# Performance work log

Measured on AMD Instinct MI355X. Metric: run time of the kernel, lower is better.

The kernel has to match this reference:

```python
import jax, jax.numpy as jnp
import numpy as np

B, S, DIMS, HEAD = 4, 4096, 1024, 16
HD = DIMS // HEAD


def setup_inputs() -> dict:
    key = jax.random.key(0)
    ks = jax.random.split(key, 9)
    inv = 1.0 / np.sqrt(DIMS)
    return {
        "x": jax.random.normal(ks[0], (B, S, DIMS), dtype=jnp.float32),
        "Wq": jax.random.normal(ks[1], (DIMS, DIMS), dtype=jnp.float32) * inv,
        "bq": jax.random.normal(ks[2], (DIMS,), dtype=jnp.float32) * 0.02,
        "Wk": jax.random.normal(ks[3], (DIMS, DIMS), dtype=jnp.float32) * inv,
        "bk": jax.random.normal(ks[4], (DIMS,), dtype=jnp.float32) * 0.02,
        "Wv": jax.random.normal(ks[5], (DIMS, DIMS), dtype=jnp.float32) * inv,
        "bv": jax.random.normal(ks[6], (DIMS,), dtype=jnp.float32) * 0.02,
        "Wo": jax.random.normal(ks[7], (DIMS, DIMS), dtype=jnp.float32) * inv,
        "bo": jax.random.normal(ks[8], (DIMS,), dtype=jnp.float32) * 0.02,
        "skip_pattern": 4,
    }


def reference(x, Wq, bq, Wk, bk, Wv, bv, Wo, bo, skip_pattern):
    b, s, _ = x.shape
    scale = DIMS ** (-0.5)  # NOTE: source scales by full dims, not head_dim

    def proj(W, bias):
        # torch Linear: x @ W.T + b ; then [B,S,H,HD] -> [B,H,S,HD]
        y = jnp.einsum('bsd,ed->bse', x, W) + bias
        return y.reshape(b, s, HEAD, HD).transpose(0, 2, 1, 3)

    q = proj(Wq, bq)
    k = proj(Wk, bk)
    v = proj(Wv, bv)

    # strided KV downsample (static python-int stride -> static shapes under jit)
    k_s = k[:, :, ::skip_pattern, :]  # [B,H,S//skip,HD]
    v_s = v[:, :, ::skip_pattern, :]

    scores = jnp.einsum('bhqd,bhkd->bhqk', q, k_s) * scale
    attn = jax.nn.softmax(scores, axis=-1)
    out = jnp.einsum('bhqk,bhkd->bhqd', attn, v_s)  # [B,H,S,HD]
    out = out.transpose(0, 2, 1, 3).reshape(b, s, DIMS)
    return jnp.einsum('bsd,ed->bse', out, Wo) + bo
```

## Files before the change

### kernel.cpp

```cpp
#include <hip/hip_runtime.h>
#include <hip/hip_bf16.h>
#include <stdint.h>


using short8 = short __attribute__((ext_vector_type(8)));
using f32x4  = float __attribute__((ext_vector_type(4)));
using f32x16 = float __attribute__((ext_vector_type(16)));

#define MFMA16(A,B,C) __builtin_amdgcn_mfma_f32_16x16x32_bf16((A),(B),(C),0,0,0)
#define MFMA32(A,B,C) __builtin_amdgcn_mfma_f32_32x32x16_bf16((A),(B),(C),0,0,0)

#define QSC 0.0450842200277800f

#define VT_OFF 4194304

__device__ __forceinline__ unsigned short f2bf(float f) {
  unsigned int x = __float_as_uint(f);
  x += 0x7fffu + ((x >> 16) & 1u);
  return (unsigned short)(x >> 16);
}

__device__ __forceinline__ unsigned pack2(float a, float b) {
  float2 t; t.x = a; t.y = b;
  union { __hip_bfloat162 h; unsigned u; } cv;
  cv.h = __float22bfloat162_rn(t);
  return cv.u;
}

__device__ __forceinline__ float fexp2(float x) {
  float r; asm("v_exp_f32 %0, %1" : "=v"(r) : "v"(x)); return r;
}

#define PLSWAP(a,b) asm volatile("v_permlane32_swap_b32 %0, %1" : "+v"(a), "+v"(b))

__device__ __forceinline__ void gld_lds16(const void* g, void* l) {
  __builtin_amdgcn_global_load_lds(
      (const __attribute__((address_space(1))) void*)g,
      (__attribute__((address_space(3))) void*)l,
      16, 0, 0);
}

__global__ __launch_bounds__(256) void cvtall_kernel(
    const float* __restrict__ x,  unsigned short* __restrict__ xb,
    const float* __restrict__ w0, const float* __restrict__ w1,
    const float* __restrict__ w2, const float* __restrict__ w3,
    unsigned short* __restrict__ o0, unsigned short* __restrict__ o1,
    unsigned short* __restrict__ o2, unsigned short* __restrict__ o3) {
  int bid = blockIdx.x, tid = threadIdx.x;
  const float* in; unsigned short* out; int n4, i0, stride;
  if (bid < 2048) {
    in = x; out = xb; n4 = 4194304; i0 = bid * 256 + tid; stride = 2048 * 256;
  } else {
    int t = (bid - 2048) >> 7;
    switch (t) {
      case 0: in = w0; out = o0; break;
      case 1: in = w1; out = o1; break;
      case 2: in = w2; out = o2; break;
      default: in = w3; out = o3; break;
    }
    n4 = 262144; i0 = ((bid - 2048) & 127) * 256 + tid; stride = 128 * 256;
  }
  for (int i = i0; i < n4; i += stride) {
    float4 v = ((const float4*)in)[i];
    ushort4 o;
    o.x = f2bf(v.x); o.y = f2bf(v.y); o.z = f2bf(v.z); o.w = f2bf(v.w);
    ((ushort4*)out)[i] = o;
  }
}

template<int MODE, int ROWMUL>
__device__ __forceinline__ void gemm_body(
    unsigned short* __restrict__ lA, unsigned short* __restrict__ lB,
    const unsigned short* __restrict__ A,
    const unsigned short* __restrict__ W,
    const float* __restrict__ biasA,
    const float* __restrict__ biasB,
    void* __restrict__ outp,
    int NB, int bid, int nwg)
{
  constexpr int K = 1024;
  int vid = (bid & 7) * (nwg >> 3) + (bid >> 3);
  int bm = vid / NB, bn = vid % NB;

  int tid = threadIdx.x;
  int w = tid >> 6, l = tid & 63;
  int wm = w >> 1, wn = w & 1;
  int fr = l & 15, fk = l >> 4;

  int sr = w * 16 + (l >> 2);
  int sc = ((l & 3) ^ ((l >> 3) & 3)) * 8;
  const unsigned short* ga0 = A + (size_t)ROWMUL * (size_t)(bm * 128 + sr) * K + sc;
  const unsigned short* ga1 = A + (size_t)ROWMUL * (size_t)(bm * 128 + 64 + sr) * K + sc;
  const unsigned short* gb0 = W + (size_t)(bn * 128 + sr) * K + sc;
  const unsigned short* gb1 = W + (size_t)(bn * 128 + 64 + sr) * K + sc;
  unsigned short* la0 = &lA[(w * 16) * 32];
  unsigned short* la1 = &lA[(64 + w * 16) * 32];
  unsigned short* lb0 = &lB[(w * 16) * 32];
  unsigned short* lb1 = &lB[(64 + w * 16) * 32];

  int physk = (fk ^ ((fr >> 1) & 3)) * 8;

  f32x4 acc[4][4];
  #pragma unroll
  for (int i = 0; i < 4; ++i)
    #pragma unroll
    for (int j = 0; j < 4; ++j) acc[i][j] = (f32x4){0.f, 0.f, 0.f, 0.f};

  for (int kt = 0; kt < K / 64; ++kt) {
    gld_lds16(ga0 + kt * 64,      la0);
    gld_lds16(ga0 + kt * 64 + 32, la0 + 4096);
    gld_lds16(ga1 + kt * 64,      la1);
    gld_lds16(ga1 + kt * 64 + 32, la1 + 4096);
    gld_lds16(gb0 + kt * 64,      lb0);
    gld_lds16(gb0 + kt * 64 + 32, lb0 + 4096);
    gld_lds16(gb1 + kt * 64,      lb1);
    gld_lds16(gb1 + kt * 64 + 32, lb1 + 4096);
    __syncthreads();
    #pragma unroll
    for (int kh = 0; kh < 2; ++kh) {
      int base = kh * 4096;
      short8 af[4], bf[4];
      #pragma unroll
      for (int mi = 0; mi < 4; ++mi)
        af[mi] = *(const short8*)&lA[base + (wm * 64 + mi * 16 + fr) * 32 + physk];
      #pragma unroll
      for (int nj = 0; nj < 4; ++nj)
        bf[nj] = *(const short8*)&lB[base + (wn * 64 + nj * 16 + fr) * 32 + physk];
      __builtin_amdgcn_s_setprio(1);
      #pragma unroll
      for (int mi = 0; mi < 4; ++mi)
        #pragma unroll
        for (int nj = 0; nj < 4; ++nj)
          acc[mi][nj] = MFMA16(af[mi], bf[nj], acc[mi][nj]);
      __builtin_amdgcn_s_setprio(0);
    }
    __syncthreads();
  }

  float bv[4];
  #pragma unroll
  for (int nj = 0; nj < 4; ++nj) {
    int n = bn * 128 + wn * 64 + nj * 16 + fr;
    bv[nj] = (MODE == 4) ? (n < 1024 ? biasA[n] : biasB[n - 1024]) : biasA[n];
  }

  #pragma unroll
  for (int mi = 0; mi < 4; ++mi) {
    #pragma unroll
    for (int nj = 0; nj < 4; ++nj) {
      #pragma unroll
      for (int j = 0; j < 4; ++j) {
        int m = bm * 128 + wm * 64 + mi * 16 + fk * 4 + j;
        int n = bn * 128 + wn * 64 + nj * 16 + fr;
        float v = acc[mi][nj][j] + bv[nj];
        if (MODE == 0) {
          ((float*)outp)[(size_t)m * 1024 + n] = v;
        } else if (MODE == 1) {
          size_t idx = (size_t)((m >> 12) * 16 + (n >> 6)) * 262144
                     + (size_t)(m & 4095) * 64 + (n & 63);
          ((unsigned short*)outp)[idx] = f2bf(v * QSC);
        } else {
          if (n < 1024) {
            size_t idx = (size_t)((m >> 10) * 16 + (n >> 6)) * 65536
                       + (size_t)(m & 1023) * 64 + (n & 63);
            ((unsigned short*)outp)[idx] = f2bf(v);
          } else {
            int nn = n - 1024;
            size_t idx = (size_t)VT_OFF
                       + (size_t)((m >> 10) * 16 + (nn >> 6)) * 65536
                       + (size_t)(nn & 63) * 1024 + (m & 1023);
            ((unsigned short*)outp)[idx] = f2bf(v);
          }
        }
      }
    }
  }
}

__global__ __launch_bounds__(256) void proj_fused_kernel(
    const unsigned short* __restrict__ xb,
    const unsigned short* __restrict__ wqb,
    const unsigned short* __restrict__ wkb,
    const float* __restrict__ bq,
    const float* __restrict__ bk,
    const float* __restrict__ bv,
    unsigned short* __restrict__ qb,
    unsigned short* __restrict__ kb)
{
  __shared__ unsigned short lA[128 * 64];
  __shared__ unsigned short lB[128 * 64];
  int bid = blockIdx.x;
  if (bid < 1024) {
    gemm_body<1, 1>(lA, lB, xb, wqb, bq, bq, qb, 8, bid, 1024);
  } else {
    gemm_body<4, 4>(lA, lB, xb, wkb, bk, bv, kb, 16, bid - 1024, 512);
  }
}

__global__ __launch_bounds__(256) void oproj_kernel(
    const unsigned short* __restrict__ ab,
    const unsigned short* __restrict__ wob,
    const float* __restrict__ bo,
    float* __restrict__ out)
{
  __shared__ unsigned short lA[128 * 64];
  __shared__ unsigned short lB[128 * 64];
  gemm_body<0, 1>(lA, lB, ab, wob, bo, bo, out, 8, blockIdx.x, 1024);
}

__global__ __launch_bounds__(512) void attn_kernel(
    const unsigned short* __restrict__ Q,
    const unsigned short* __restrict__ Ks,
    const unsigned short* __restrict__ Vt,
    unsigned short* __restrict__ O)
{
  __shared__ unsigned short lds[16384];
  unsigned short* lsK = lds;
  unsigned short* lsV = lds + 8192;

  int bid = blockIdx.x;
  int vid = (bid & 7) * 128 + (bid >> 3);
  int bh = vid >> 4;
  int qt = vid & 15;
  int tid = threadIdx.x;
  int w = tid >> 6, l = tid & 63;
  int l31 = l & 31, hi = l >> 5;
  int q0 = qt * 256 + w * 32;

  short8 qf[4];
  {
    const unsigned short* qp = Q + ((size_t)bh * 4096 + q0 + l31) * 64 + hi * 8;
    #pragma unroll
    for (int s = 0; s < 4; ++s) qf[s] = *(const short8*)(qp + s * 16);
  }

  const unsigned short* Kbh = Ks + (size_t)bh * 65536;
  const unsigned short* Vbh = Vt + (size_t)bh * 65536;

  int r = w * 8 + (l >> 3);
  int c0 = ((l & 7) ^ (l >> 3)) * 8;
  int dst = w * 512;

#define STAGE(BUF, KC)                                                          \
  {                                                                             \
    const unsigned short* Kb = Kbh + (KC) * 4096;                               \
    const unsigned short* Vb = Vbh + (KC) * 64;                                 \
    gld_lds16(Kb + r * 64 + c0, &lsK[(BUF) * 4096 + dst]);                      \
    gld_lds16(Vb + (size_t)r * 1024 + c0, &lsV[(BUF) * 4096 + dst]);            \
  }

  float lrun = 0.f;
  f32x16 oa0, oa1;
  #pragma unroll
  for (int rr = 0; rr < 16; ++rr) { oa0[rr] = 0.f; oa1[rr] = 0.f; }

  STAGE(0, 0);
  __syncthreads();

  int rb0 = l31 * 64, rb1 = rb0 + 2048;
  int rsw = l31 & 7;

  for (int kc = 0; kc < 16; ++kc) {
    int b = kc & 1;
    if (kc + 1 < 16) STAGE(b ^ 1, kc + 1);

    const unsigned short* Kl = &lsK[b * 4096];
    const unsigned short* Vl = &lsV[b * 4096];

    f32x16 s0, s1;
    #pragma unroll
    for (int rr = 0; rr < 16; ++rr) { s0[rr] = 0.f; s1[rr] = 0.f; }
    __builtin_amdgcn_s_setprio(1);
    #pragma unroll
    for (int s = 0; s < 4; ++s) {
      int co = ((hi + 2 * s) ^ rsw) * 8;
      short8 kf0 = *(const short8*)&Kl[rb0 + co];
      short8 kf1 = *(const short8*)&Kl[rb1 + co];
      s0 = MFMA32(kf0, qf[s], s0);
      s1 = MFMA32(kf1, qf[s], s1);
    }
    __builtin_amdgcn_s_setprio(0);

    unsigned pk0[8], pk1[8];
    float sm0 = 0.f, sm1 = 0.f, sm2 = 0.f, sm3 = 0.f;
    #pragma unroll
    for (int i = 0; i < 4; ++i) {
      float a = fexp2(s0[2*i]), bb = fexp2(s0[2*i+1]);
      sm0 += a + bb; pk0[i] = pack2(a, bb);
    }
    #pragma unroll
    for (int i = 4; i < 8; ++i) {
      float a = fexp2(s0[2*i]), bb = fexp2(s0[2*i+1]);
      sm1 += a + bb; pk0[i] = pack2(a, bb);
    }
    #pragma unroll
    for (int i = 0; i < 4; ++i) {
      float a = fexp2(s1[2*i]), bb = fexp2(s1[2*i+1]);
      sm2 += a + bb; pk1[i] = pack2(a, bb);
    }
    #pragma unroll
    for (int i = 4; i < 8; ++i) {
      float a = fexp2(s1[2*i]), bb = fexp2(s1[2*i+1]);
      sm3 += a + bb; pk1[i] = pack2(a, bb);
    }
    lrun += (sm0 + sm1) + (sm2 + sm3);

    short8 pf[4];
    #pragma unroll
    for (int half = 0; half < 2; ++half) {
      #pragma unroll
      for (int sl = 0; sl < 2; ++sl) {
        unsigned a0 = half ? pk1[sl*4+0] : pk0[sl*4+0];
        unsigned a1 = half ? pk1[sl*4+1] : pk0[sl*4+1];
        unsigned b0 = half ? pk1[sl*4+2] : pk0[sl*4+2];
        unsigned b1 = half ? pk1[sl*4+3] : pk0[sl*4+3];
        unsigned t0 = a0; PLSWAP(t0, b0);
        unsigned t1 = a1; PLSWAP(t1, b1);
        union { unsigned u[4]; short8 s8; } u;
        u.u[0] = t0;
        u.u[1] = t1;
        u.u[2] = b0;
        u.u[3] = b1;
        pf[half * 2 + sl] = u.s8;
      }
    }

    __builtin_amdgcn_s_setprio(1);
    #pragma unroll
    for (int s = 0; s < 4; ++s) {
      int co = ((hi + 2 * s) ^ rsw) * 8;
      short8 vf0 = *(const short8*)&Vl[rb0 + co];
      short8 vf1 = *(const short8*)&Vl[rb1 + co];
      oa0 = MFMA32(vf0, pf[s], oa0);
      oa1 = MFMA32(vf1, pf[s], oa1);
    }
    __builtin_amdgcn_s_setprio(0);

    __syncthreads();
  }
#undef STAGE

  lrun += __shfl_xor(lrun, 32);
  float inv = 1.0f / lrun;

  unsigned short* ob = lds + w * 2048;
  #pragma unroll
  for (int dblk = 0; dblk < 2; ++dblk) {
    #pragma unroll
    for (int rr = 0; rr < 16; ++rr) {
      float v = (dblk ? oa1[rr] : oa0[rr]) * inv;
      int d = dblk * 32 + (rr & 3) + 8 * (rr >> 2) + 4 * hi;
      ob[l31 * 64 + (d ^ ((l31 & 7) << 3))] = f2bf(v);
    }
  }
  int b = bh >> 4, h = bh & 15;
  #pragma unroll
  for (int pass = 0; pass < 8; ++pass) {
    int qq = pass * 4 + (l >> 4);
    int cc = (l & 15) * 4;
    ushort4 vv = *(const ushort4*)&ob[qq * 64 + (cc ^ ((qq & 7) << 3))];
    *(ushort4*)&O[((size_t)b * 4096 + q0 + qq) * 1024 + h * 64 + cc] = vv;
  }
}

extern "C" void kernel_launch(void* const* d_in, const int* in_sizes, int n_in,
                              void* d_out, int out_size, void* d_ws, size_t ws_size,
                              hipStream_t stream) {
  const float* x  = (const float*)d_in[0];
  const float* Wq = (const float*)d_in[1];
  const float* bq = (const float*)d_in[2];
  const float* Wk = (const float*)d_in[3];
  const float* bk = (const float*)d_in[4];
  const float* Wv = (const float*)d_in[5];
  const float* bv = (const float*)d_in[6];
  const float* Wo = (const float*)d_in[7];
  const float* bo = (const float*)d_in[8];
  float* out = (float*)d_out;

  unsigned short* ws  = (unsigned short*)d_ws;
  unsigned short* xb  = ws;
  unsigned short* wqb = xb  + 16777216;
  unsigned short* wkb = wqb + 1048576;
  unsigned short* wvb = wkb + 1048576;
  unsigned short* wob = wvb + 1048576;
  unsigned short* qb  = wob + 1048576;
  unsigned short* kb  = qb  + 16777216;
  unsigned short* vtb = kb  + 4194304;
  unsigned short* ab  = vtb + 4194304;

  cvtall_kernel<<<2560, 256, 0, stream>>>(x, xb, Wq, Wk, Wv, Wo, wqb, wkb, wvb, wob);
  proj_fused_kernel<<<1536, 256, 0, stream>>>(xb, wqb, wkb, bq, bk, bv, qb, kb);
  attn_kernel<<<1024, 512, 0, stream>>>(qb, kb, vtb, ab);
  oproj_kernel<<<1024, 256, 0, stream>>>(ab, wob, bo, out);
}
```

Before: 230.9 us.

## Double-buffer LDS tiles in projection GEMMs to overlap loads with MFMA

Converts the GEMM main loop to a two-stage LDS double buffer: the next k-tile is issued via global-to-LDS loads before computing on the current buffer, with one barrier per iteration. This is meant to hide global memory latency behind MFMA work. LDS usage per block doubles to 64KB, which may reduce occupancy. There is no explicit wait on the async loads before the barrier, so correctness depends on the barrier implying a vmcnt wait.

```diff
diff --git a/kernel.cpp b/kernel.cpp
--- a/kernel.cpp
+++ b/kernel.cpp
@@ -93,10 +93,8 @@
   const unsigned short* ga1 = A + (size_t)ROWMUL * (size_t)(bm * 128 + 64 + sr) * K + sc;
   const unsigned short* gb0 = W + (size_t)(bn * 128 + sr) * K + sc;
   const unsigned short* gb1 = W + (size_t)(bn * 128 + 64 + sr) * K + sc;
-  unsigned short* la0 = &lA[(w * 16) * 32];
-  unsigned short* la1 = &lA[(64 + w * 16) * 32];
-  unsigned short* lb0 = &lB[(w * 16) * 32];
-  unsigned short* lb1 = &lB[(64 + w * 16) * 32];
+  int la0 = (w * 16) * 32;
+  int la1 = (64 + w * 16) * 32;
 
   int physk = (fk ^ ((fr >> 1) & 3)) * 8;
 
@@ -106,19 +104,29 @@
     #pragma unroll
     for (int j = 0; j < 4; ++j) acc[i][j] = (f32x4){0.f, 0.f, 0.f, 0.f};
 
+#define GSTAGE(BUF, KT)                                                         \
+  {                                                                             \
+    int o = (BUF) * 8192;                                                       \
+    gld_lds16(ga0 + (KT) * 64,      &lA[o + la0]);                              \
+    gld_lds16(ga0 + (KT) * 64 + 32, &lA[o + la0 + 4096]);                       \
+    gld_lds16(ga1 + (KT) * 64,      &lA[o + la1]);                              \
+    gld_lds16(ga1 + (KT) * 64 + 32, &lA[o + la1 + 4096]);                       \
+    gld_lds16(gb0 + (KT) * 64,      &lB[o + la0]);                              \
+    gld_lds16(gb0 + (KT) * 64 + 32, &lB[o + la0 + 4096]);                       \
+    gld_lds16(gb1 + (KT) * 64,      &lB[o + la1]);                              \
+    gld_lds16(gb1 + (KT) * 64 + 32, &lB[o + la1 + 4096]);                       \
+  }
+
+  GSTAGE(0, 0);
+  __syncthreads();
+
   for (int kt = 0; kt < K / 64; ++kt) {
-    gld_lds16(ga0 + kt * 64,      la0);
-    gld_lds16(ga0 + kt * 64 + 32, la0 + 4096);
-    gld_lds16(ga1 + kt * 64,      la1);
-    gld_lds16(ga1 + kt * 64 + 32, la1 + 4096);
-    gld_lds16(gb0 + kt * 64,      lb0);
-    gld_lds16(gb0 + kt * 64 + 32, lb0 + 4096);
-    gld_lds16(gb1 + kt * 64,      lb1);
-    gld_lds16(gb1 + kt * 64 + 32, lb1 + 4096);
-    __syncthreads();
+    int b = kt & 1;
+    if (kt + 1 < K / 64) GSTAGE(b ^ 1, kt + 1);
+
     #pragma unroll
     for (int kh = 0; kh < 2; ++kh) {
-      int base = kh * 4096;
+      int base = b * 8192 + kh * 4096;
       short8 af[4], bf[4];
       #pragma unroll
       for (int mi = 0; mi < 4; ++mi)
@@ -136,6 +144,7 @@
     }
     __syncthreads();
   }
+#undef GSTAGE
 
   float bv[4];
   #pragma unroll
@@ -187,8 +196,8 @@
     unsigned short* __restrict__ qb,
     unsigned short* __restrict__ kb)
 {
-  __shared__ unsigned short lA[128 * 64];
-  __shared__ unsigned short lB[128 * 64];
+  __shared__ unsigned short lA[2 * 8192];
+  __shared__ unsigned short lB[2 * 8192];
   int bid = blockIdx.x;
   if (bid < 1024) {
     gemm_body<1, 1>(lA, lB, xb, wqb, bq, bq, qb, 8, bid, 1024);
@@ -203,8 +212,8 @@
     const float* __restrict__ bo,
     float* __restrict__ out)
 {
-  __shared__ unsigned short lA[128 * 64];
-  __shared__ unsigned short lB[128 * 64];
+  __shared__ unsigned short lA[2 * 8192];
+  __shared__ unsigned short lB[2 * 8192];
   gemm_body<0, 1>(lA, lB, ab, wob, bo, bo, out, 8, blockIdx.x, 1024);
 }
 
```

Result: faster. 226.2 us (-2.0%).
